# Kernel optimization log

Hardware: AMD Instinct MI355X
Metric: run time of the kernel (lower is better)

## Reference

```python
import jax, jax.numpy as jnp
import numpy as np


def setup_inputs() -> dict:
    key = jax.random.key(0)
    k1, k2, k3, k4 = jax.random.split(key, 4)
    M, K, N = 64, 8192, 28672
    group_size = 128
    num_groups = K // group_size  # 64
    x = jax.random.normal(k1, (M, K), dtype=jnp.float16)
    # packed int4: each int32 holds one byte value in [0, 256) = two 4-bit nibbles
    weight_packed = jax.random.randint(k2, (N, K // 2), 0, 256, dtype=jnp.int32)
    # small positive per-group scales, typical of int4 quantization
    scales = (jax.random.uniform(k3, (N, num_groups), dtype=jnp.float16) * jnp.float16(0.02)
              + jnp.float16(0.001))
    bias = jax.random.normal(k4, (N,), dtype=jnp.float16) * jnp.float16(0.1)
    return {"x": x, "weight_packed": weight_packed, "scales": scales,
            "bias": bias, "group_size": group_size}


def reference(x, weight_packed, scales, bias, group_size):
    # x: [M, K] fp16; weight_packed: [N, K//2] bytes; scales: [N, K//group_size] fp16
    N, Khalf = weight_packed.shape
    K = 2 * Khalf
    num_groups = K // group_size
    # unpack nibbles: low nibble = even K index, high nibble = odd K index
    low = weight_packed & 0xF
    high = (weight_packed >> 4) & 0xF
    w_int = jnp.stack([low, high], axis=-1).reshape(N, K)  # [N, K] in [0, 16)
    # dequantize with zero-point 8 and per-group scales
    w = (w_int.astype(jnp.float16) - jnp.float16(8.0)).reshape(N, num_groups, group_size)
    w = (w * scales[:, :, None]).reshape(N, K)  # [N, K] fp16
    out = jnp.einsum("mk,nk->mn", x, w)  # [M, N] fp16
    return out + bias[None, :]
```

## Files before the change

### kernel.cpp

```cpp
#include <hip/hip_runtime.h>
#include <stdint.h>


typedef __attribute__((ext_vector_type(8))) short     short8;
typedef __attribute__((ext_vector_type(4))) float     f32x4;
typedef __attribute__((ext_vector_type(4))) int       i32x4;
typedef __attribute__((ext_vector_type(2))) _Float16  f16x2;
typedef __attribute__((ext_vector_type(8))) _Float16  f16x8;

static __device__ __forceinline__ void gload_lds16(const void* gp, void* lp) {
    __builtin_amdgcn_global_load_lds(
        (const __attribute__((address_space(1))) unsigned int*)gp,
        (__attribute__((address_space(3))) unsigned int*)lp, 16, 0, 0);
}

static __device__ __forceinline__ f16x8 dequant(const i32x4& w, f16x2 s2) {
    const f16x2 c1032 = {(_Float16)1032.0f, (_Float16)1032.0f};
    union { unsigned u[4]; f16x8 v; } r;
    #pragma unroll
    for (int j = 0; j < 4; ++j) {
        unsigned v = (unsigned)w[j];
        unsigned u = ((v & 0xFu) | 0x64006400u) | ((v << 12) & 0xF0000u);
        f16x2 h = __builtin_bit_cast(f16x2, u);
        h = (h - c1032) * s2;
        r.u[j] = __builtin_bit_cast(unsigned, h);
    }
    return r.v;
}

__global__ __launch_bounds__(256)
void xpack_kernel(const float* __restrict__ x, unsigned short* __restrict__ xf, int K) {
    int c    = blockIdx.x * 256 + threadIdx.x;
    int g    = c >> 10;
    int st   = (c >> 8) & 3;
    int mt   = (c >> 6) & 3;
    int lane = c & 63;
    int quad = lane >> 4, l15 = lane & 15;
    const float* p = x + (size_t)(l15 + mt * 16) * K + g * 128 + st * 32 + quad * 8;
    f32x4 lo = *(const f32x4*)p;
    f32x4 hi = *(const f32x4*)(p + 4);
    f16x8 r = { (_Float16)lo[0], (_Float16)lo[1], (_Float16)lo[2], (_Float16)lo[3],
                (_Float16)hi[0], (_Float16)hi[1], (_Float16)hi[2], (_Float16)hi[3] };
    *(short8*)(xf + (size_t)c * 8) = __builtin_bit_cast(short8, r);
}

__global__ __launch_bounds__(256)
void int4mm_kernel(const unsigned short* __restrict__ xf,
                   const int*   __restrict__ wp,
                   const float* __restrict__ sc,
                   const float* __restrict__ bias,
                   float*       __restrict__ out,
                   int K, int N)
{
    __shared__ char lds[49152];
    char*  ldsW = lds;
    float* ldsS = (float*)(lds + 32768);

    const int tid  = threadIdx.x;
    const int lane = tid & 63;
    const int wave = tid >> 6;
    const int quad = lane >> 4;
    const int l15  = lane & 15;
    const int blk64 = blockIdx.x * 64;
    const int ng   = K / 128;

    const char* wp8 = (const char*)wp;

    unsigned woff[4];
    #pragma unroll
    for (int j = 0; j < 4; ++j) {
        int cloc  = wave * 16 + j * 4 + quad;
        int chunk = l15 ^ (j * 4 + quad);
        woff[j] = ((unsigned)(blk64 + cloc) << 14) + ((unsigned)chunk << 4);
    }

    int rdW[4];
    #pragma unroll
    for (int nt = 0; nt < 4; ++nt)
        rdW[nt] = (nt * 16 + l15) * 256 + (((wave * 4 + quad) ^ l15) << 4);

    {
        const int c  = tid & 63;
        const int g0 = (tid >> 6) * 16;
        const float* sp = sc + (size_t)(blk64 + c) * ng + g0;
        f32x4 s0 = *(const f32x4*)(sp);
        f32x4 s1 = *(const f32x4*)(sp + 4);
        f32x4 s2 = *(const f32x4*)(sp + 8);
        f32x4 s3 = *(const f32x4*)(sp + 12);
        #pragma unroll
        for (int j = 0; j < 4; ++j) {
            ldsS[(g0 + 0  + j) * 64 + c] = s0[j];
            ldsS[(g0 + 4  + j) * 64 + c] = s1[j];
            ldsS[(g0 + 8  + j) * 64 + c] = s2[j];
            ldsS[(g0 + 12 + j) * 64 + c] = s3[j];
        }
    }
    #pragma unroll
    for (int j = 0; j < 4; ++j)
        gload_lds16(wp8 + woff[j], ldsW + (wave * 4 + j) * 1024);

    const char* xbase = (const char*)xf + wave * 4096 + lane * 16;
    f16x8 xn[4], xc[4];
    #pragma unroll
    for (int mt = 0; mt < 4; ++mt)
        xn[mt] = *(const f16x8*)(xbase + mt * 1024);

    f32x4 acc[4][4];
    #pragma unroll
    for (int mt = 0; mt < 4; ++mt)
        #pragma unroll
        for (int nt = 0; nt < 4; ++nt)
            acc[mt][nt] = f32x4{0.f, 0.f, 0.f, 0.f};

    __syncthreads();

    #pragma unroll 1
    for (int g = 0; g < ng; ++g) {
        const int p  = g & 1;
        const int gn = (g + 1 < ng) ? g + 1 : ng - 1;

        #pragma unroll
        for (int mt = 0; mt < 4; ++mt) xc[mt] = xn[mt];

        const char* xs = xbase + (size_t)gn * 16384;
        #pragma unroll
        for (int mt = 0; mt < 4; ++mt)
            xn[mt] = *(const f16x8*)(xs + mt * 1024);

        __builtin_amdgcn_s_barrier();

        #pragma unroll
        for (int j = 0; j < 4; ++j)
            gload_lds16(wp8 + woff[j] + (size_t)gn * 256,
                        ldsW + (p ^ 1) * 16384 + (wave * 4 + j) * 1024);

        asm volatile("s_waitcnt vmcnt(8)" ::: "memory");
        __builtin_amdgcn_s_barrier();
        __builtin_amdgcn_sched_barrier(0);

        const char* wb = ldsW + p * 16384;
        i32x4 v0 = *(const i32x4*)(wb + rdW[0]);
        i32x4 v1 = *(const i32x4*)(wb + rdW[1]);
        i32x4 v2 = *(const i32x4*)(wb + rdW[2]);
        i32x4 v3 = *(const i32x4*)(wb + rdW[3]);

        const float* sg = ldsS + g * 64;
        const float sf0 = sg[l15], sf1 = sg[16 + l15];
        const float sf2 = sg[32 + l15], sf3 = sg[48 + l15];

        {
            f16x8 b = dequant(v0, f16x2{(_Float16)sf0, (_Float16)sf0});
            #pragma unroll
            for (int mt = 0; mt < 4; ++mt)
                acc[mt][0] = __builtin_amdgcn_mfma_f32_16x16x32_f16(xc[mt], b, acc[mt][0], 0, 0, 0);
        }
        {
            f16x8 b = dequant(v1, f16x2{(_Float16)sf1, (_Float16)sf1});
            #pragma unroll
            for (int mt = 0; mt < 4; ++mt)
                acc[mt][1] = __builtin_amdgcn_mfma_f32_16x16x32_f16(xc[mt], b, acc[mt][1], 0, 0, 0);
        }
        {
            f16x8 b = dequant(v2, f16x2{(_Float16)sf2, (_Float16)sf2});
            #pragma unroll
            for (int mt = 0; mt < 4; ++mt)
                acc[mt][2] = __builtin_amdgcn_mfma_f32_16x16x32_f16(xc[mt], b, acc[mt][2], 0, 0, 0);
        }
        {
            f16x8 b = dequant(v3, f16x2{(_Float16)sf3, (_Float16)sf3});
            #pragma unroll
            for (int mt = 0; mt < 4; ++mt)
                acc[mt][3] = __builtin_amdgcn_mfma_f32_16x16x32_f16(xc[mt], b, acc[mt][3], 0, 0, 0);
        }
    }

    __syncthreads();
    #pragma unroll
    for (int o = 0; o < 4; ++o) {
        if (o == wave) continue;
        const int s = wave - (wave > o ? 1 : 0);
        #pragma unroll
        for (int nt = 0; nt < 4; ++nt)
            *(f32x4*)(lds + (size_t)(((o * 3 + s) * 4 + nt) * 1024) + lane * 16)
                = acc[o][nt];
    }
    __syncthreads();

    f32x4 own[4];
    #pragma unroll
    for (int nt = 0; nt < 4; ++nt) own[nt] = acc[0][nt];
    #pragma unroll
    for (int o = 1; o < 4; ++o)
        if (wave == o) {
            own[0] = acc[o][0]; own[1] = acc[o][1];
            own[2] = acc[o][2]; own[3] = acc[o][3];
        }
    #pragma unroll
    for (int s = 0; s < 3; ++s)
        #pragma unroll
        for (int nt = 0; nt < 4; ++nt)
            own[nt] += *(const f32x4*)(lds + (size_t)(((wave * 3 + s) * 4 + nt) * 1024)
                                       + lane * 16);

    #pragma unroll
    for (int nt = 0; nt < 4; ++nt) {
        const int col = blk64 + nt * 16 + l15;
        const float bv = bias[col];
        #pragma unroll
        for (int r = 0; r < 4; ++r)
            out[(size_t)(wave * 16 + quad * 4 + r) * N + col] = own[nt][r] + bv;
    }
}

extern "C" void kernel_launch(void* const* d_in, const int* in_sizes, int n_in,
                              void* d_out, int out_size, void* d_ws, size_t ws_size,
                              hipStream_t stream)
{
    const float* x    = (const float*)d_in[0];
    const int*   wp   = (const int*)d_in[1];
    const float* sc   = (const float*)d_in[2];
    const float* bias = (const float*)d_in[3];
    float*       out  = (float*)d_out;

    const int N  = in_sizes[3];
    const long long Kh = (long long)in_sizes[1] / N;
    const int K  = (int)(2 * Kh);
    const int ng = K / 128;

    unsigned short* xf = (unsigned short*)d_ws;

    xpack_kernel<<<(ng * 1024) / 256, 256, 0, stream>>>(x, xf, K);
    int4mm_kernel<<<N / 64, 256, 0, stream>>>(xf, wp, sc, bias, out, K, N);
}
```

Measured before the change: 107.2 us.

## Deepen weight pipeline to four LDS stages with nontemporal loads

Replaces the double-buffered weight LDS pipeline with a four-slot ring that keeps three groups of weight loads in flight. The main loop is unrolled by four with four register sets of prefetched activations, each issued four groups ahead. Weight loads now carry a nontemporal cache hint, and launch bounds request two blocks per CU. The aim is to hide more HBM latency for this memory-bound GEMV-like kernel, at the cost of more LDS (80KB) and registers, which may limit occupancy; the loop also now assumes the group count is a multiple of four.

```diff
diff --git a/kernel.cpp b/kernel.cpp
--- a/kernel.cpp
+++ b/kernel.cpp
@@ -8,10 +8,10 @@
 typedef __attribute__((ext_vector_type(2))) _Float16  f16x2;
 typedef __attribute__((ext_vector_type(8))) _Float16  f16x8;
 
-static __device__ __forceinline__ void gload_lds16(const void* gp, void* lp) {
+static __device__ __forceinline__ void gload_lds16_nt(const void* gp, void* lp) {
     __builtin_amdgcn_global_load_lds(
         (const __attribute__((address_space(1))) unsigned int*)gp,
-        (__attribute__((address_space(3))) unsigned int*)lp, 16, 0, 0);
+        (__attribute__((address_space(3))) unsigned int*)lp, 16, 0, 2);
 }
 
 static __device__ __forceinline__ f16x8 dequant(const i32x4& w, f16x2 s2) {
@@ -44,7 +44,7 @@
     *(short8*)(xf + (size_t)c * 8) = __builtin_bit_cast(short8, r);
 }
 
-__global__ __launch_bounds__(256)
+__global__ __launch_bounds__(256, 2)
 void int4mm_kernel(const unsigned short* __restrict__ xf,
                    const int*   __restrict__ wp,
                    const float* __restrict__ sc,
@@ -52,9 +52,9 @@
                    float*       __restrict__ out,
                    int K, int N)
 {
-    __shared__ char lds[49152];
+    __shared__ char lds[81920];
     char*  ldsW = lds;
-    float* ldsS = (float*)(lds + 32768);
+    float* ldsS = (float*)(lds + 65536);
 
     const int tid  = threadIdx.x;
     const int lane = tid & 63;
@@ -69,15 +69,16 @@
     unsigned woff[4];
     #pragma unroll
     for (int j = 0; j < 4; ++j) {
-        int cloc  = wave * 16 + j * 4 + quad;
-        int chunk = l15 ^ (j * 4 + quad);
+        const int cloc  = wave * 16 + j * 4 + quad;
+        const int chunk = l15 ^ (j * 4 + quad);
         woff[j] = ((unsigned)(blk64 + cloc) << 14) + ((unsigned)chunk << 4);
     }
 
+    const int q = wave * 4 + quad;
     int rdW[4];
     #pragma unroll
     for (int nt = 0; nt < 4; ++nt)
-        rdW[nt] = (nt * 16 + l15) * 256 + (((wave * 4 + quad) ^ l15) << 4);
+        rdW[nt] = (nt * 16 + l15) * 256 + ((q ^ l15) << 4);
 
     {
         const int c  = tid & 63;
@@ -96,14 +97,21 @@
         }
     }
     #pragma unroll
-    for (int j = 0; j < 4; ++j)
-        gload_lds16(wp8 + woff[j], ldsW + (wave * 4 + j) * 1024);
+    for (int g = 0; g < 3; ++g)
+        #pragma unroll
+        for (int j = 0; j < 4; ++j)
+            gload_lds16_nt(wp8 + woff[j] + (size_t)g * 256,
+                           ldsW + g * 16384 + (wave * 4 + j) * 1024);
 
     const char* xbase = (const char*)xf + wave * 4096 + lane * 16;
-    f16x8 xn[4], xc[4];
-    #pragma unroll
-    for (int mt = 0; mt < 4; ++mt)
-        xn[mt] = *(const f16x8*)(xbase + mt * 1024);
+    f16x8 xA[4], xB[4], xC[4], xD[4];
+    #pragma unroll
+    for (int mt = 0; mt < 4; ++mt) {
+        xA[mt] = *(const f16x8*)(xbase +         mt * 1024);
+        xB[mt] = *(const f16x8*)(xbase + 16384 + mt * 1024);
+        xC[mt] = *(const f16x8*)(xbase + 32768 + mt * 1024);
+        xD[mt] = *(const f16x8*)(xbase + 49152 + mt * 1024);
+    }
 
     f32x4 acc[4][4];
     #pragma unroll
@@ -114,65 +122,69 @@
 
     __syncthreads();
 
+#define SUBITER(J, SLOTC, SLOTS, XS)                                          \
+    {                                                                         \
+        const int j_  = (J);                                                  \
+        const int gw  = (j_ + 3 < ng) ? j_ + 3 : ng - 1;                      \
+        const int gx  = (j_ + 4 < ng) ? j_ + 4 : ng - 1;                      \
+        __builtin_amdgcn_s_barrier();                                         \
+        _Pragma("unroll")                                                     \
+        for (int j2 = 0; j2 < 4; ++j2)                                        \
+            gload_lds16_nt(wp8 + woff[j2] + (size_t)gw * 256,                 \
+                           ldsW + (SLOTS) * 16384 + (wave * 4 + j2) * 1024);  \
+        asm volatile("s_waitcnt vmcnt(24)" ::: "memory");                     \
+        __builtin_amdgcn_s_barrier();                                         \
+        __builtin_amdgcn_sched_barrier(0);                                    \
+        const char* wb_ = ldsW + (SLOTC) * 16384;                             \
+        i32x4 v0_ = *(const i32x4*)(wb_ + rdW[0]);                            \
+        i32x4 v1_ = *(const i32x4*)(wb_ + rdW[1]);                            \
+        i32x4 v2_ = *(const i32x4*)(wb_ + rdW[2]);                            \
+        i32x4 v3_ = *(const i32x4*)(wb_ + rdW[3]);                            \
+        const float* sg_ = ldsS + j_ * 64;                                    \
+        const float sf0_ = sg_[l15],      sf1_ = sg_[16 + l15];               \
+        const float sf2_ = sg_[32 + l15], sf3_ = sg_[48 + l15];               \
+        {                                                                     \
+            f16x8 b_ = dequant(v0_, f16x2{(_Float16)sf0_, (_Float16)sf0_});   \
+            _Pragma("unroll")                                                 \
+            for (int mt = 0; mt < 4; ++mt)                                    \
+                acc[mt][0] = __builtin_amdgcn_mfma_f32_16x16x32_f16(          \
+                                 XS[mt], b_, acc[mt][0], 0, 0, 0);            \
+        }                                                                     \
+        {                                                                     \
+            f16x8 b_ = dequant(v1_, f16x2{(_Float16)sf1_, (_Float16)sf1_});   \
+            _Pragma("unroll")                                                 \
+            for (int mt = 0; mt < 4; ++mt)                                    \
+                acc[mt][1] = __builtin_amdgcn_mfma_f32_16x16x32_f16(          \
+                                 XS[mt], b_, acc[mt][1], 0, 0, 0);            \
+        }                                                                     \
+        {                                                                     \
+            f16x8 b_ = dequant(v2_, f16x2{(_Float16)sf2_, (_Float16)sf2_});   \
+            _Pragma("unroll")                                                 \
+            for (int mt = 0; mt < 4; ++mt)                                    \
+                acc[mt][2] = __builtin_amdgcn_mfma_f32_16x16x32_f16(          \
+                                 XS[mt], b_, acc[mt][2], 0, 0, 0);            \
+        }                                                                     \
+        {                                                                     \
+            f16x8 b_ = dequant(v3_, f16x2{(_Float16)sf3_, (_Float16)sf3_});   \
+            _Pragma("unroll")                                                 \
+            for (int mt = 0; mt < 4; ++mt)                                    \
+                acc[mt][3] = __builtin_amdgcn_mfma_f32_16x16x32_f16(          \
+                                 XS[mt], b_, acc[mt][3], 0, 0, 0);            \
+        }                                                                     \
+        const char* xs_ = xbase + (size_t)gx * 16384;                         \
+        _Pragma("unroll")                                                     \
+        for (int mt = 0; mt < 4; ++mt)                                        \
+            XS[mt] = *(const f16x8*)(xs_ + mt * 1024);                        \
+    }
+
     #pragma unroll 1
-    for (int g = 0; g < ng; ++g) {
-        const int p  = g & 1;
-        const int gn = (g + 1 < ng) ? g + 1 : ng - 1;
-
-        #pragma unroll
-        for (int mt = 0; mt < 4; ++mt) xc[mt] = xn[mt];
-
-        const char* xs = xbase + (size_t)gn * 16384;
-        #pragma unroll
-        for (int mt = 0; mt < 4; ++mt)
-            xn[mt] = *(const f16x8*)(xs + mt * 1024);
-
-        __builtin_amdgcn_s_barrier();
-
-        #pragma unroll
-        for (int j = 0; j < 4; ++j)
-            gload_lds16(wp8 + woff[j] + (size_t)gn * 256,
-                        ldsW + (p ^ 1) * 16384 + (wave * 4 + j) * 1024);
-
-        asm volatile("s_waitcnt vmcnt(8)" ::: "memory");
-        __builtin_amdgcn_s_barrier();
-        __builtin_amdgcn_sched_barrier(0);
-
-        const char* wb = ldsW + p * 16384;
-        i32x4 v0 = *(const i32x4*)(wb + rdW[0]);
-        i32x4 v1 = *(const i32x4*)(wb + rdW[1]);
-        i32x4 v2 = *(const i32x4*)(wb + rdW[2]);
-        i32x4 v3 = *(const i32x4*)(wb + rdW[3]);
-
-        const float* sg = ldsS + g * 64;
-        const float sf0 = sg[l15], sf1 = sg[16 + l15];
-        const float sf2 = sg[32 + l15], sf3 = sg[48 + l15];
-
-        {
-            f16x8 b = dequant(v0, f16x2{(_Float16)sf0, (_Float16)sf0});
-            #pragma unroll
-            for (int mt = 0; mt < 4; ++mt)
-                acc[mt][0] = __builtin_amdgcn_mfma_f32_16x16x32_f16(xc[mt], b, acc[mt][0], 0, 0, 0);
-        }
-        {
-            f16x8 b = dequant(v1, f16x2{(_Float16)sf1, (_Float16)sf1});
-            #pragma unroll
-            for (int mt = 0; mt < 4; ++mt)
-                acc[mt][1] = __builtin_amdgcn_mfma_f32_16x16x32_f16(xc[mt], b, acc[mt][1], 0, 0, 0);
-        }
-        {
-            f16x8 b = dequant(v2, f16x2{(_Float16)sf2, (_Float16)sf2});
-            #pragma unroll
-            for (int mt = 0; mt < 4; ++mt)
-                acc[mt][2] = __builtin_amdgcn_mfma_f32_16x16x32_f16(xc[mt], b, acc[mt][2], 0, 0, 0);
-        }
-        {
-            f16x8 b = dequant(v3, f16x2{(_Float16)sf3, (_Float16)sf3});
-            #pragma unroll
-            for (int mt = 0; mt < 4; ++mt)
-                acc[mt][3] = __builtin_amdgcn_mfma_f32_16x16x32_f16(xc[mt], b, acc[mt][3], 0, 0, 0);
-        }
-    }
+    for (int g4 = 0; g4 < ng; g4 += 4) {
+        SUBITER(g4 + 0, 0, 3, xA)
+        SUBITER(g4 + 1, 1, 0, xB)
+        SUBITER(g4 + 2, 2, 1, xC)
+        SUBITER(g4 + 3, 3, 2, xD)
+    }
+#undef SUBITER
 
     __syncthreads();
     #pragma unroll
```

New measurement: 115.0 us. +7.3%, slower.

## Split K across two blocks per N tile and add a reduction kernel

Applied to the files above, without the earlier changes.

Splits the K dimension in two so each 64-column tile is handled by two blocks. Each block writes its partial sums to a workspace buffer, and a new reduce kernel adds the two partials plus the bias. This raises the block count from 448 to 896 so the GPU's compute units are better filled. It also adds a launch-bounds occupancy hint and a nontemporal cache policy on the weight loads. The cost is an extra kernel launch and an extra write and read of partial outputs to global memory, and it falls back to the single-pass path when the workspace is too small.

```diff
diff --git a/kernel.cpp b/kernel.cpp
--- a/kernel.cpp
+++ b/kernel.cpp
@@ -8,10 +8,10 @@
 typedef __attribute__((ext_vector_type(2))) _Float16  f16x2;
 typedef __attribute__((ext_vector_type(8))) _Float16  f16x8;
 
-static __device__ __forceinline__ void gload_lds16(const void* gp, void* lp) {
+static __device__ __forceinline__ void gload_lds16_nt(const void* gp, void* lp) {
     __builtin_amdgcn_global_load_lds(
         (const __attribute__((address_space(1))) unsigned int*)gp,
-        (__attribute__((address_space(3))) unsigned int*)lp, 16, 0, 0);
+        (__attribute__((address_space(3))) unsigned int*)lp, 16, 0, 2);
 }
 
 static __device__ __forceinline__ f16x8 dequant(const i32x4& w, f16x2 s2) {
@@ -45,12 +45,23 @@
 }
 
 __global__ __launch_bounds__(256)
+void reduce_kernel(const float* __restrict__ pbuf, const float* __restrict__ bias,
+                   float* __restrict__ out, int N, int total) {
+    int i = (blockIdx.x * 256 + threadIdx.x) * 4;
+    if (i >= total) return;
+    f32x4 a = *(const f32x4*)(pbuf + i);
+    f32x4 b = *(const f32x4*)(pbuf + (size_t)total + i);
+    f32x4 bb = *(const f32x4*)(bias + (i % N));
+    *(f32x4*)(out + i) = (a + b) + bb;
+}
+
+__global__ __launch_bounds__(256, 3)
 void int4mm_kernel(const unsigned short* __restrict__ xf,
                    const int*   __restrict__ wp,
                    const float* __restrict__ sc,
                    const float* __restrict__ bias,
-                   float*       __restrict__ out,
-                   int K, int N)
+                   float*       __restrict__ dst,
+                   int K, int N, int nsplit)
 {
     __shared__ char lds[49152];
     char*  ldsW = lds;
@@ -61,49 +72,57 @@
     const int wave = tid >> 6;
     const int quad = lane >> 4;
     const int l15  = lane & 15;
-    const int blk64 = blockIdx.x * 64;
     const int ng   = K / 128;
+    const int gps  = ng / nsplit;
+    const int bid  = blockIdx.x;
+    const int ntile = bid / nsplit;
+    const int ks    = bid - ntile * nsplit;
+    const int blk64 = ntile * 64;
+    const int g0    = ks * gps;
 
     const char* wp8 = (const char*)wp;
 
     unsigned woff[4];
     #pragma unroll
     for (int j = 0; j < 4; ++j) {
-        int cloc  = wave * 16 + j * 4 + quad;
-        int chunk = l15 ^ (j * 4 + quad);
-        woff[j] = ((unsigned)(blk64 + cloc) << 14) + ((unsigned)chunk << 4);
-    }
-
+        const int cloc  = wave * 16 + j * 4 + quad;
+        const int chunk = l15 ^ (j * 4 + quad);
+        woff[j] = ((unsigned)(blk64 + cloc) << 14) + ((unsigned)chunk << 4)
+                + (unsigned)g0 * 256;
+    }
+
+    const int q = wave * 4 + quad;
     int rdW[4];
     #pragma unroll
     for (int nt = 0; nt < 4; ++nt)
-        rdW[nt] = (nt * 16 + l15) * 256 + (((wave * 4 + quad) ^ l15) << 4);
+        rdW[nt] = (nt * 16 + l15) * 256 + ((q ^ l15) << 4);
 
     {
-        const int c  = tid & 63;
-        const int g0 = (tid >> 6) * 16;
-        const float* sp = sc + (size_t)(blk64 + c) * ng + g0;
-        f32x4 s0 = *(const f32x4*)(sp);
-        f32x4 s1 = *(const f32x4*)(sp + 4);
-        f32x4 s2 = *(const f32x4*)(sp + 8);
-        f32x4 s3 = *(const f32x4*)(sp + 12);
-        #pragma unroll
-        for (int j = 0; j < 4; ++j) {
-            ldsS[(g0 + 0  + j) * 64 + c] = s0[j];
-            ldsS[(g0 + 4  + j) * 64 + c] = s1[j];
-            ldsS[(g0 + 8  + j) * 64 + c] = s2[j];
-            ldsS[(g0 + 12 + j) * 64 + c] = s3[j];
+        const int c   = tid & 63;
+        const int gg0 = (tid >> 6) * (gps >> 2);
+        const float* sp = sc + (size_t)(blk64 + c) * ng + g0 + gg0;
+        #pragma unroll
+        for (int b = 0; b < 4; ++b) {
+            if (b < (gps >> 4) || (b == 0)) {
+            }
+        }
+        const int nb = gps >> 4;
+        for (int b = 0; b < nb; ++b) {
+            f32x4 s = *(const f32x4*)(sp + b * 4);
+            #pragma unroll
+            for (int j = 0; j < 4; ++j)
+                ldsS[(gg0 + b * 4 + j) * 64 + c] = s[j];
         }
     }
     #pragma unroll
     for (int j = 0; j < 4; ++j)
-        gload_lds16(wp8 + woff[j], ldsW + (wave * 4 + j) * 1024);
+        gload_lds16_nt(wp8 + woff[j], ldsW + (wave * 4 + j) * 1024);
 
     const char* xbase = (const char*)xf + wave * 4096 + lane * 16;
     f16x8 xn[4], xc[4];
     #pragma unroll
     for (int mt = 0; mt < 4; ++mt)
-        xn[mt] = *(const f16x8*)(xbase + mt * 1024);
+        xn[mt] = *(const f16x8*)(xbase + (size_t)g0 * 16384 + mt * 1024);
 
     f32x4 acc[4][4];
     #pragma unroll
@@ -115,14 +134,13 @@
     __syncthreads();
 
     #pragma unroll 1
-    for (int g = 0; g < ng; ++g) {
+    for (int g = 0; g < gps; ++g) {
         const int p  = g & 1;
-        const int gn = (g + 1 < ng) ? g + 1 : ng - 1;
+        const int gn = (g + 1 < gps) ? g + 1 : gps - 1;
 
         #pragma unroll
         for (int mt = 0; mt < 4; ++mt) xc[mt] = xn[mt];
-
-        const char* xs = xbase + (size_t)gn * 16384;
+        const char* xs = xbase + (size_t)(g0 + gn) * 16384;
         #pragma unroll
         for (int mt = 0; mt < 4; ++mt)
             xn[mt] = *(const f16x8*)(xs + mt * 1024);
@@ -131,23 +149,23 @@
 
         #pragma unroll
         for (int j = 0; j < 4; ++j)
-            gload_lds16(wp8 + woff[j] + (size_t)gn * 256,
-                        ldsW + (p ^ 1) * 16384 + (wave * 4 + j) * 1024);
+            gload_lds16_nt(wp8 + woff[j] + (size_t)gn * 256,
+                           ldsW + (p ^ 1) * 16384 + (wave * 4 + j) * 1024);
 
         asm volatile("s_waitcnt vmcnt(8)" ::: "memory");
         __builtin_amdgcn_s_barrier();
         __builtin_amdgcn_sched_barrier(0);
 
         const char* wb = ldsW + p * 16384;
+        const float* sg = ldsS + g * 64;
+        const float sf0 = sg[l15], sf1 = sg[16 + l15];
+        const float sf2 = sg[32 + l15], sf3 = sg[48 + l15];
+
         i32x4 v0 = *(const i32x4*)(wb + rdW[0]);
         i32x4 v1 = *(const i32x4*)(wb + rdW[1]);
         i32x4 v2 = *(const i32x4*)(wb + rdW[2]);
         i32x4 v3 = *(const i32x4*)(wb + rdW[3]);
 
-        const float* sg = ldsS + g * 64;
-        const float sf0 = sg[l15], sf1 = sg[16 + l15];
-        const float sf2 = sg[32 + l15], sf3 = sg[48 + l15];
-
         {
             f16x8 b = dequant(v0, f16x2{(_Float16)sf0, (_Float16)sf0});
             #pragma unroll
@@ -202,13 +220,14 @@
             own[nt] += *(const f32x4*)(lds + (size_t)(((wave * 3 + s) * 4 + nt) * 1024)
                                        + lane * 16);
 
+    float* obase = dst + (size_t)ks * 64 * N;
     #pragma unroll
     for (int nt = 0; nt < 4; ++nt) {
         const int col = blk64 + nt * 16 + l15;
-        const float bv = bias[col];
+        const float bv = bias ? bias[col] : 0.0f;
         #pragma unroll
         for (int r = 0; r < 4; ++r)
-            out[(size_t)(wave * 16 + quad * 4 + r) * N + col] = own[nt][r] + bv;
+            obase[(size_t)(wave * 16 + quad * 4 + r) * N + col] = own[nt][r] + bv;
     }
 }
 
@@ -228,7 +247,19 @@
     const int ng = K / 128;
 
     unsigned short* xf = (unsigned short*)d_ws;
+    const size_t xf_bytes = (size_t)ng * 16384;
+    const int    total    = 64 * N;
+    const size_t need     = xf_bytes + 2ull * total * 4ull;
 
     xpack_kernel<<<(ng * 1024) / 256, 256, 0, stream>>>(x, xf, K);
-    int4mm_kernel<<<N / 64, 256, 0, stream>>>(xf, wp, sc, bias, out, K, N);
-}
+
+    if (ws_size >= need && (ng & 31) == 0) {
+        float* pbuf = (float*)((char*)d_ws + xf_bytes);
+        int4mm_kernel<<<(N / 64) * 2, 256, 0, stream>>>(xf, wp, sc, nullptr, pbuf,
+                                                        K, N, 2);
+        reduce_kernel<<<(total / 4 + 255) / 256, 256, 0, stream>>>(pbuf, bias, out,
+                                                                   N, total);
+    } else {
+        int4mm_kernel<<<N / 64, 256, 0, stream>>>(xf, wp, sc, bias, out, K, N, 1);
+    }
+}
```

Result: slower. 126.5 us (+18.1%).
